# Performance work log

Hardware: AMD Instinct MI355X
Metric: run time of the kernel (lower is better)

The kernel has to match this reference:

```python
import jax, jax.numpy as jnp
import numpy as np

B, S, N, Q, H, Z = 2, 4096, 256, 64, 8, 512

def _glorot(key, shape):
    fan_in, fan_out = shape[-2], shape[-1]
    limit = np.sqrt(6.0 / (fan_in + fan_out))
    return jax.random.uniform(key, shape, jnp.float32, -limit, limit)

def setup_inputs() -> dict:
    key = jax.random.key(0)
    k0, k1, k2, k3 = jax.random.split(key, 4)
    X = jax.random.normal(k0, (B, S, N), dtype=jnp.float32)
    M = _glorot(k1, (H, N, N))        # stacked per-head bilinear matrices
    W_v = _glorot(k2, (H, N, Q))      # stacked per-head value projections
    W0 = _glorot(k3, (Q * H, Z))      # output projection
    return {"X": X, "M": M, "W_v": W_v, "W0": W0}

def reference(X, M, W_v, W0):
    # scores[b,h,s,t] = (X @ M_h @ X^T)[b,s,t] / q   (source divides by q, not sqrt(q))
    q = W_v.shape[-1]
    XM = jnp.einsum('bsn,hnm->bhsm', X, M)
    scores = jnp.einsum('bhsm,btm->bhst', XM, X) / q      # [B,H,S,S]
    A = jax.nn.softmax(scores, axis=-1)
    V = jnp.einsum('btn,hnq->bhtq', X, W_v)               # [B,H,S,Q]
    Zh = jnp.einsum('bhst,bhtq->bshq', A, V)              # [B,S,H,Q]
    Zc = Zh.reshape(Zh.shape[0], Zh.shape[1], -1)         # concat heads -> [B,S,H*Q]
    return Zc @ W0                                        # [B,S,Z]
```

## Files before the change

kernel.cpp:

```cpp
#include <hip/hip_runtime.h>

typedef unsigned short u16;
typedef unsigned long long uptr;
typedef __attribute__((ext_vector_type(8))) short bf16x8;
typedef __attribute__((ext_vector_type(4))) float f32x4;
typedef __attribute__((ext_vector_type(16))) float f32x16;

#define MFMA16(a,b,c) __builtin_amdgcn_mfma_f32_16x16x32_bf16((a),(b),(c),0,0,0)
#define MFMA32(a,b,c) __builtin_amdgcn_mfma_f32_32x32x16_bf16((a),(b),(c),0,0,0)

#define BB 2
#define SS 4096
#define NN 256
#define HH 8
#define QQ 64
#define ZZ 512

__device__ __forceinline__ u16 f2bf(float f){
  unsigned int u = __float_as_uint(f);
  u += 0x7fffu + ((u >> 16) & 1u);
  return (u16)(u >> 16);
}

__device__ __forceinline__ f32x4 fzero(){ f32x4 z = {0.f,0.f,0.f,0.f}; return z; }

__device__ __forceinline__ f32x16 zero16(){
  f32x16 z;
  #pragma unroll
  for (int i = 0; i < 16; i++) z[i] = 0.f;
  return z;
}

__device__ __forceinline__ unsigned pkbf(float a, float b){
  unsigned r;
  asm("v_cvt_pk_bf16_f32 %0, %1, %2" : "=v"(r) : "v"(a), "v"(b));
  return r;
}

typedef __attribute__((address_space(1))) const void gas_void;
typedef __attribute__((address_space(3))) void las_void;
__device__ __forceinline__ void gload16(const void* g, void* l){
  __builtin_amdgcn_global_load_lds((gas_void*)(uptr)g,
                                   (las_void*)(uptr)(unsigned)(uptr)l, 16, 0, 0);
}

__device__ __forceinline__ void do_transpose(const float* __restrict__ ip,
                                             u16* __restrict__ op, int R, int C,
                                             int bx, int by, float (*t)[33], int tid){
  int c0 = bx * 32, r0 = by * 32;
  int c = tid & 31, r = tid >> 5;
  #pragma unroll
  for (int rr = 0; rr < 32; rr += 8)
    t[r + rr][c] = ip[(size_t)(r0 + r + rr) * C + (c0 + c)];
  __syncthreads();
  #pragma unroll
  for (int rr = 0; rr < 32; rr += 8)
    op[(size_t)(c0 + r + rr) * R + (r0 + c)] = f2bf(t[c][r + rr]);
}

__global__ __launch_bounds__(256) void prep_kernel(const float* __restrict__ X,
                                                   const float* __restrict__ M,
                                                   const float* __restrict__ Wv,
                                                   const float* __restrict__ W0,
                                                   u16* __restrict__ Kb,
                                                   u16* __restrict__ Mq,
                                                   u16* __restrict__ Wvt,
                                                   u16* __restrict__ W0t){
  __shared__ float t[32][33];
  int bid = blockIdx.x, tid = threadIdx.x;
  if (bid < 2048){
    int i = bid * 256 + tid;
    float4 v = ((const float4*)X)[i];
    ushort4 o;
    o.x = f2bf(v.x); o.y = f2bf(v.y); o.z = f2bf(v.z); o.w = f2bf(v.w);
    ((ushort4*)Kb)[i] = o;
    return;
  }
  int b2 = bid - 2048;
  if (b2 < 64){
    int h = b2 >> 3, ct = b2 & 7;
    const float* Msrc = M + (size_t)h * NN * NN;
    u16* dst = Mq + (size_t)(h * 8 + ct) * 8192;
    #pragma unroll
    for (int rep = 0; rep < 4; rep++){
      int p = rep * 256 + tid;
      int kk = p >> 6, lane = p & 63;
      int l31 = lane & 31, hi = lane >> 5;
      const float* s = Msrc + (size_t)(kk * 16 + hi * 8) * NN + ct * 32 + l31;
      union { u16 u[8]; uint4 v; } tmp;
      #pragma unroll
      for (int j = 0; j < 8; j++) tmp.u[j] = f2bf(s[(size_t)j * NN]);
      *(uint4*)(dst + (size_t)p * 8) = tmp.v;
    }
    return;
  }
  if (b2 < 192){
    int b3 = b2 - 64;
    int bz = b3 >> 4, by = (b3 >> 1) & 7, bx = b3 & 1;
    do_transpose(Wv + (size_t)bz * NN * QQ, Wvt + (size_t)bz * NN * QQ, NN, QQ, bx, by, t, tid);
  } else {
    int b4 = b2 - 192;
    int by = b4 >> 4, bx = b4 & 15;
    do_transpose(W0, W0t, ZZ, ZZ, bx, by, t, tid);
  }
}

__global__ __launch_bounds__(256) void vt_kernel(const u16* __restrict__ Xb,
                                                 const u16* __restrict__ Wvt,
                                                 u16* __restrict__ Vt){
  int bh = blockIdx.y, b = bh >> 3, h = bh & 7;
  int tbase = blockIdx.x * 256;
  int lane = threadIdx.x & 63, w = threadIdx.x >> 6;
  int lr = lane & 15, g = lane >> 4, lk = g * 8;

  const u16* Ap = Wvt + ((size_t)h * QQ + w * 16 + lr) * NN + lk;
  bf16x8 afr[8];
  #pragma unroll
  for (int ks = 0; ks < 8; ks++) afr[ks] = *(const bf16x8*)(Ap + 32 * ks);

  f32x4 acc[16];
  #pragma unroll
  for (int n = 0; n < 16; n++) acc[n] = fzero();

  for (int n = 0; n < 16; n++){
    const u16* bp = Xb + ((size_t)b * SS + tbase + n * 16 + lr) * NN + lk;
    #pragma unroll
    for (int ks = 0; ks < 8; ks++)
      acc[n] = MFMA16(afr[ks], *(const bf16x8*)(bp + 32 * ks), acc[n]);
  }
  u16* Op = Vt + ((size_t)bh * QQ + w * 16 + g * 4) * SS + tbase;
  #pragma unroll
  for (int n = 0; n < 16; n++)
    #pragma unroll
    for (int r = 0; r < 4; r++)
      Op[(size_t)r * SS + n * 16 + lr] = f2bf(acc[n][r]);
}

__global__ __launch_bounds__(256, 2) void attn_kernel(const u16* __restrict__ Mq,
                                                      const u16* __restrict__ Kb,
                                                      const u16* __restrict__ Vt,
                                                      u16* __restrict__ Zc){
  int lid = blockIdx.x;
  int bh = (lid & 7) | (((lid >> 3) & 1) << 3);
  int qi = lid >> 4;
  int b = bh >> 3, h = bh & 7;

  int tid = threadIdx.x, lane = tid & 63, w = tid >> 6;
  int l31 = lane & 31, hi = lane >> 5;
  int hi16 = hi * 16;
  int sw = (lane & 7) << 4;

  __shared__ u16 k_lds[2 * 64 * 256];
  __shared__ u16 v_lds[2 * 64 * 64];
  char* kl = (char*)k_lds;
  char* vl = (char*)v_lds;

  int qrow = qi * 128 + w * 32 + l31;

  const char* Kg = (const char*)(Kb + (size_t)b * SS * NN);
  const char* Vg = (const char*)(Vt + (size_t)bh * QQ * SS);

  int koffK[8], koffV[2];
  #pragma unroll
  for (int c = 0; c < 8; c++){
    int x = c * 4096 + w * 1024 + lane * 16;
    koffK[c] = x ^ (((x >> 9) & 7) << 4);
  }
  #pragma unroll
  for (int c = 0; c < 2; c++){
    int x = c * 4096 + w * 1024 + lane * 16;
    int vq = x >> 7, ko = x & 127;
    koffV[c] = vq * 8192 + (ko ^ ((vq & 7) << 4));
  }
  int kOff[16], vOff[4];
  #pragma unroll
  for (int ks = 0; ks < 16; ks++) kOff[ks] = l31 * 512 + ((ks * 32 + hi16) ^ sw);
  #pragma unroll
  for (int c = 0; c < 4; c++) vOff[c] = l31 * 128 + ((c * 32 + hi16) ^ sw);

#define STAGE(kt_, CUR_) do {                                              \
    const char* kg_ = Kg + (size_t)(kt_) * 32768;                          \
    const char* vg_ = Vg + (size_t)(kt_) * 128;                            \
    _Pragma("unroll")                                                      \
    for (int c = 0; c < 8; c++)                                            \
      gload16(kg_ + koffK[c], kl + (CUR_) * 32768 + c * 4096 + w * 1024);  \
    _Pragma("unroll")                                                      \
    for (int c = 0; c < 2; c++)                                            \
      gload16(vg_ + koffV[c], vl + (CUR_) * 8192 + c * 4096 + w * 1024);   \
  } while (0)

  STAGE(0, 0);

  bf16x8 qfr[16];
  {
    const float QSCALE = 0.015625f * 1.4426950408889634f;
    const u16* Xp = Kb + ((size_t)b * SS + qrow) * NN + hi * 8;
    bf16x8 xfr[16];
    #pragma unroll
    for (int kk = 0; kk < 16; kk++) xfr[kk] = *(const bf16x8*)(Xp + kk * 16);
    const u16* Mqh = Mq + (size_t)(h * 8) * 8192 + (size_t)lane * 8;
    #pragma unroll
    for (int ct = 0; ct < 8; ct++){
      f32x16 acc = zero16();
      const u16* ap = Mqh + (size_t)ct * 8192;
      #pragma unroll
      for (int kk = 0; kk < 16; kk++)
        acc = MFMA32(*(const bf16x8*)(ap + kk * 512), xfr[kk], acc);
      #pragma unroll
      for (int i = 0; i < 16; i++) acc[i] *= QSCALE;
      {
        unsigned a0 = pkbf(acc[0], acc[1]),  b0 = pkbf(acc[2], acc[3]);
        unsigned c0 = pkbf(acc[4], acc[5]),  d0 = pkbf(acc[6], acc[7]);
        asm("v_permlane32_swap_b32 %0, %1" : "+v"(a0), "+v"(c0));
        asm("v_permlane32_swap_b32 %0, %1" : "+v"(b0), "+v"(d0));
        union { bf16x8 v; unsigned u[4]; } u0;
        u0.u[0] = a0; u0.u[1] = b0; u0.u[2] = c0; u0.u[3] = d0;
        qfr[2 * ct] = u0.v;
      }
      {
        unsigned a1 = pkbf(acc[8], acc[9]),   b1 = pkbf(acc[10], acc[11]);
        unsigned c1 = pkbf(acc[12], acc[13]), d1 = pkbf(acc[14], acc[15]);
        asm("v_permlane32_swap_b32 %0, %1" : "+v"(a1), "+v"(c1));
        asm("v_permlane32_swap_b32 %0, %1" : "+v"(b1), "+v"(d1));
        union { bf16x8 v; unsigned u[4]; } u1;
        u1.u[0] = a1; u1.u[1] = b1; u1.u[2] = c1; u1.u[3] = d1;
        qfr[2 * ct + 1] = u1.v;
      }
    }
  }

  f32x16 o0 = zero16(), o1 = zero16();
  float m = -1e30f, l = 0.f;

#define PVSTEP(P, RB, VOFF, VCONST) do {                                   \
    unsigned a_ = pkbf(P[RB+0], P[RB+1]);                                  \
    unsigned b_ = pkbf(P[RB+2], P[RB+3]);                                  \
    unsigned c_ = pkbf(P[RB+4], P[RB+5]);                                  \
    unsigned d_ = pkbf(P[RB+6], P[RB+7]);                                  \
    asm("v_permlane32_swap_b32 %0, %1" : "+v"(a_), "+v"(c_));              \
    asm("v_permlane32_swap_b32 %0, %1" : "+v"(b_), "+v"(d_));              \
    union { bf16x8 v; unsigned u[4]; } pu_;                                \
    pu_.u[0] = a_; pu_.u[1] = b_; pu_.u[2] = c_; pu_.u[3] = d_;            \
    bf16x8 vf0_ = *(const bf16x8*)(vl + (VOFF) + (VCONST));                \
    bf16x8 vf1_ = *(const bf16x8*)(vl + (VOFF) + (VCONST) + 4096);         \
    o0 = MFMA32(pu_.v, vf0_, o0);                                          \
    o1 = MFMA32(pu_.v, vf1_, o1);                                          \
  } while (0)

#define ITER(kt_, CUR_, LAST_) do {                                        \
    if (!(LAST_)) STAGE((kt_) + 1, (CUR_) ^ 1);                            \
    if (LAST_) { asm volatile("s_waitcnt vmcnt(0)" ::: "memory"); }        \
    else       { asm volatile("s_waitcnt vmcnt(10)" ::: "memory"); }       \
    __builtin_amdgcn_sched_barrier(0);                                     \
    __builtin_amdgcn_s_barrier();                                          \
    __builtin_amdgcn_sched_barrier(0);                                     \
    f32x16 p0 = zero16(), p1 = zero16();                                   \
    __builtin_amdgcn_s_setprio(1);                                         \
    _Pragma("unroll")                                                      \
    for (int ks = 0; ks < 16; ks++){                                       \
      bf16x8 k0 = *(const bf16x8*)(kl + (CUR_) * 32768 + kOff[ks]);        \
      bf16x8 k1 = *(const bf16x8*)(kl + (CUR_) * 32768 + kOff[ks] + 16384);\
      p0 = MFMA32(k0, qfr[ks], p0);                                        \
      p1 = MFMA32(k1, qfr[ks], p1);                                        \
    }                                                                      \
    __builtin_amdgcn_s_setprio(0);                                         \
      \
    float r_[16];                                                          \
    _Pragma("unroll")                                                      \
    for (int i = 0; i < 16; i++) r_[i] = fmaxf(p0[i], p1[i]);              \
    _Pragma("unroll")                                                      \
    for (int i = 0; i < 8; i++) r_[i] = fmaxf(r_[i], r_[i + 8]);           \
    _Pragma("unroll")                                                      \
    for (int i = 0; i < 4; i++) r_[i] = fmaxf(r_[i], r_[i + 4]);           \
    float pm = fmaxf(fmaxf(r_[0], r_[1]), fmaxf(r_[2], r_[3]));            \
    pm = fmaxf(pm, __shfl_xor(pm, 32));                                    \
    if (__any(pm > m + 8.0f)){                        \
      float mn_ = fmaxf(m, pm);                                            \
      float fs_ = exp2f(m - mn_);                                          \
      m = mn_; l *= fs_;                                                   \
      _Pragma("unroll")                                                    \
      for (int i = 0; i < 16; i++){                                        \
        int q_ = (i & 3) + 8 * (i >> 2) + 4 * hi;                          \
        float fv_ = __int_as_float(__builtin_amdgcn_ds_bpermute(           \
                        q_ << 2, __float_as_int(fs_)));                    \
        o0[i] *= fv_; o1[i] *= fv_;                                        \
      }                                                                    \
    }                                                                      \
    _Pragma("unroll")                                                      \
    for (int i = 0; i < 16; i++){                                          \
      p0[i] = exp2f(p0[i] - m);                                            \
      p1[i] = exp2f(p1[i] - m);                                            \
    }                                                                      \
    { float s_[16];                                                        \
      _Pragma("unroll")                                                    \
      for (int i = 0; i < 16; i++) s_[i] = p0[i] + p1[i];                  \
      _Pragma("unroll")                                                    \
      for (int i = 0; i < 8; i++) s_[i] += s_[i + 8];                      \
      _Pragma("unroll")                                                    \
      for (int i = 0; i < 4; i++) s_[i] += s_[i + 4];                      \
      float ps_ = (s_[0] + s_[1]) + (s_[2] + s_[3]);                       \
      ps_ += __shfl_xor(ps_, 32);                                          \
      l += ps_; }                                                          \
    __builtin_amdgcn_s_setprio(1);                                         \
    PVSTEP(p0, 0, vOff[0], (CUR_) * 8192);                                 \
    PVSTEP(p0, 8, vOff[1], (CUR_) * 8192);                                 \
    PVSTEP(p1, 0, vOff[2], (CUR_) * 8192);                                 \
    PVSTEP(p1, 8, vOff[3], (CUR_) * 8192);                                 \
    __builtin_amdgcn_s_setprio(0);                                         \
    __builtin_amdgcn_s_barrier();                                          \
    __builtin_amdgcn_sched_barrier(0);                                     \
  } while (0)

  for (int kt2 = 0; kt2 < 31; kt2++){
    ITER(2 * kt2,     0, 0);
    ITER(2 * kt2 + 1, 1, 0);
  }
  ITER(62, 0, 0);
  ITER(63, 1, 1);
#undef ITER
#undef PVSTEP
#undef STAGE

  float inv = 1.0f / l;
  u16* Op = Zc + ((size_t)b * SS + qi * 128 + w * 32) * (HH * QQ) + h * QQ;
  #pragma unroll
  for (int i = 0; i < 16; i++){
    int q = (i & 3) + 8 * (i >> 2) + 4 * hi;
    float fv = __int_as_float(__builtin_amdgcn_ds_bpermute(q << 2, __float_as_int(inv)));
    u16* row = Op + (size_t)q * (HH * QQ);
    row[l31]      = f2bf(o0[i] * fv);
    row[32 + l31] = f2bf(o1[i] * fv);
  }
}

__global__ __launch_bounds__(256) void out_kernel(const u16* __restrict__ Zc,
                                                  const u16* __restrict__ W0t,
                                                  float* __restrict__ out){
  int rbase = blockIdx.x * 64, cbase = blockIdx.y * 128;
  int lane = threadIdx.x & 63, w = threadIdx.x >> 6;
  int lr = lane & 15, g = lane >> 4, lk = g * 8;

  const u16* Ap = Zc + (size_t)(rbase + w * 16 + lr) * ZZ + lk;
  f32x4 acc[8];
  #pragma unroll
  for (int n = 0; n < 8; n++) acc[n] = fzero();

  for (int ks = 0; ks < 16; ks++){
    bf16x8 afr = *(const bf16x8*)(Ap + 32 * ks);
    #pragma unroll
    for (int n = 0; n < 8; n++){
      const u16* bp = W0t + (size_t)(cbase + n * 16 + lr) * ZZ + lk + 32 * ks;
      acc[n] = MFMA16(afr, *(const bf16x8*)bp, acc[n]);
    }
  }
  float* Op = out + (size_t)(rbase + w * 16 + g * 4) * ZZ + cbase;
  #pragma unroll
  for (int n = 0; n < 8; n++)
    #pragma unroll
    for (int r = 0; r < 4; r++)
      Op[(size_t)r * ZZ + n * 16 + lr] = acc[n][r];
}

extern "C" void kernel_launch(void* const* d_in, const int* in_sizes, int n_in,
                              void* d_out, int out_size, void* d_ws, size_t ws_size,
                              hipStream_t stream){
  (void)in_sizes; (void)n_in; (void)out_size; (void)ws_size;
  const float* X  = (const float*)d_in[0];
  const float* M  = (const float*)d_in[1];
  const float* Wv = (const float*)d_in[2];
  const float* W0 = (const float*)d_in[3];
  float* out = (float*)d_out;

  char* ws = (char*)d_ws;
  size_t off = 0;
  auto alloc = [&](size_t bytes) -> void* {
    void* p = ws + off; off += (bytes + 255) & ~(size_t)255; return p;
  };
  u16* Kb  = (u16*)alloc((size_t)BB * SS * NN * 2);
  u16* Vtb = (u16*)alloc((size_t)BB * HH * QQ * SS * 2);
  u16* Mq  = (u16*)alloc((size_t)HH * NN * NN * 2);
  u16* Wvt = (u16*)alloc((size_t)HH * QQ * NN * 2);
  u16* W0t = (u16*)alloc((size_t)ZZ * ZZ * 2);
  u16* Zc  = (u16*)alloc((size_t)BB * SS * HH * QQ * 2);

  prep_kernel<<<dim3(2496), dim3(256), 0, stream>>>(X, M, Wv, W0, Kb, Mq, Wvt, W0t);
  vt_kernel<<<dim3(SS/256, BB*HH), dim3(256), 0, stream>>>(Kb, Wvt, Vtb);
  attn_kernel<<<dim3(512), dim3(256), 0, stream>>>(Mq, Kb, Vtb, Zc);
  out_kernel<<<dim3(BB*SS/64, ZZ/128), dim3(256), 0, stream>>>(Zc, W0t, out);
}
```

Baseline: 344.5 us.

## Shrink attention blocks, drop double buffering, stage operands through LDS

The attention kernel moves to 128-thread blocks covering 64 query rows with a single-buffered K/V LDS tile. The grid doubles to 1024 blocks and up to four blocks may share a CU. Loads now wait on vmcnt(0) before compute and the next tile is issued only after the compute finishes, so load latency is no longer overlapped within a block. vt_kernel and out_kernel now stage their X/Zc tiles into swizzled LDS with async global-to-LDS loads instead of reading fragments directly from global memory, and vt_kernel uses half the rows per block.

```diff
diff --git a/kernel.cpp b/kernel.cpp
--- a/kernel.cpp
+++ b/kernel.cpp
@@ -108,35 +108,51 @@
 __global__ __launch_bounds__(256) void vt_kernel(const u16* __restrict__ Xb,
                                                  const u16* __restrict__ Wvt,
                                                  u16* __restrict__ Vt){
+  __shared__ u16 x_lds[128 * 256];
   int bh = blockIdx.y, b = bh >> 3, h = bh & 7;
-  int tbase = blockIdx.x * 256;
-  int lane = threadIdx.x & 63, w = threadIdx.x >> 6;
+  int tbase = blockIdx.x * 128;
+  int tid = threadIdx.x;
+  int lane = tid & 63, w = tid >> 6;
   int lr = lane & 15, g = lane >> 4, lk = g * 8;
+
+  const char* src = (const char*)(Xb + ((size_t)b * SS + tbase) * NN);
+  #pragma unroll
+  for (int c = 0; c < 16; c++){
+    int x = c * 4096 + tid * 16;
+    gload16(src + (x ^ (((x >> 9) & 7) << 4)), (char*)x_lds + x);
+  }
 
   const u16* Ap = Wvt + ((size_t)h * QQ + w * 16 + lr) * NN + lk;
   bf16x8 afr[8];
   #pragma unroll
   for (int ks = 0; ks < 8; ks++) afr[ks] = *(const bf16x8*)(Ap + 32 * ks);
 
-  f32x4 acc[16];
-  #pragma unroll
-  for (int n = 0; n < 16; n++) acc[n] = fzero();
-
-  for (int n = 0; n < 16; n++){
-    const u16* bp = Xb + ((size_t)b * SS + tbase + n * 16 + lr) * NN + lk;
-    #pragma unroll
-    for (int ks = 0; ks < 8; ks++)
-      acc[n] = MFMA16(afr[ks], *(const bf16x8*)(bp + 32 * ks), acc[n]);
+  asm volatile("s_waitcnt vmcnt(0)" ::: "memory");
+  __syncthreads();
+
+  f32x4 acc[8];
+  #pragma unroll
+  for (int n = 0; n < 8; n++) acc[n] = fzero();
+
+  #pragma unroll
+  for (int n = 0; n < 8; n++){
+    int row = n * 16 + lr;
+    int rb = row * 512, swr = (row & 7) << 4;
+    #pragma unroll
+    for (int ks = 0; ks < 8; ks++){
+      bf16x8 xf = *(const bf16x8*)((const char*)x_lds + ((rb + lk * 2 + 64 * ks) ^ swr));
+      acc[n] = MFMA16(afr[ks], xf, acc[n]);
+    }
   }
   u16* Op = Vt + ((size_t)bh * QQ + w * 16 + g * 4) * SS + tbase;
   #pragma unroll
-  for (int n = 0; n < 16; n++)
+  for (int n = 0; n < 8; n++)
     #pragma unroll
     for (int r = 0; r < 4; r++)
       Op[(size_t)r * SS + n * 16 + lr] = f2bf(acc[n][r]);
 }
 
-__global__ __launch_bounds__(256, 2) void attn_kernel(const u16* __restrict__ Mq,
+__global__ __launch_bounds__(128, 4) void attn_kernel(const u16* __restrict__ Mq,
                                                       const u16* __restrict__ Kb,
                                                       const u16* __restrict__ Vt,
                                                       u16* __restrict__ Zc){
@@ -150,25 +166,25 @@
   int hi16 = hi * 16;
   int sw = (lane & 7) << 4;
 
-  __shared__ u16 k_lds[2 * 64 * 256];
-  __shared__ u16 v_lds[2 * 64 * 64];
+  __shared__ u16 k_lds[64 * 256];
+  __shared__ u16 v_lds[64 * 64];
   char* kl = (char*)k_lds;
   char* vl = (char*)v_lds;
 
-  int qrow = qi * 128 + w * 32 + l31;
+  int qrow = qi * 64 + w * 32 + l31;
 
   const char* Kg = (const char*)(Kb + (size_t)b * SS * NN);
   const char* Vg = (const char*)(Vt + (size_t)bh * QQ * SS);
 
-  int koffK[8], koffV[2];
-  #pragma unroll
-  for (int c = 0; c < 8; c++){
-    int x = c * 4096 + w * 1024 + lane * 16;
+  int koffK[16], koffV[4];
+  #pragma unroll
+  for (int c = 0; c < 16; c++){
+    int x = c * 2048 + tid * 16;
     koffK[c] = x ^ (((x >> 9) & 7) << 4);
   }
   #pragma unroll
-  for (int c = 0; c < 2; c++){
-    int x = c * 4096 + w * 1024 + lane * 16;
+  for (int c = 0; c < 4; c++){
+    int x = c * 2048 + tid * 16;
     int vq = x >> 7, ko = x & 127;
     koffV[c] = vq * 8192 + (ko ^ ((vq & 7) << 4));
   }
@@ -178,18 +194,18 @@
   #pragma unroll
   for (int c = 0; c < 4; c++) vOff[c] = l31 * 128 + ((c * 32 + hi16) ^ sw);
 
-#define STAGE(kt_, CUR_) do {                                              \
+#define STAGE(kt_) do {                                                    \
     const char* kg_ = Kg + (size_t)(kt_) * 32768;                          \
     const char* vg_ = Vg + (size_t)(kt_) * 128;                            \
     _Pragma("unroll")                                                      \
-    for (int c = 0; c < 8; c++)                                            \
-      gload16(kg_ + koffK[c], kl + (CUR_) * 32768 + c * 4096 + w * 1024);  \
-    _Pragma("unroll")                                                      \
-    for (int c = 0; c < 2; c++)                                            \
-      gload16(vg_ + koffV[c], vl + (CUR_) * 8192 + c * 4096 + w * 1024);   \
+    for (int c = 0; c < 16; c++)                                           \
+      gload16(kg_ + koffK[c], kl + c * 2048 + tid * 16);                   \
+    _Pragma("unroll")                                                      \
+    for (int c = 0; c < 4; c++)                                            \
+      gload16(vg_ + koffV[c], vl + c * 2048 + tid * 16);                   \
   } while (0)
 
-  STAGE(0, 0);
+  STAGE(0);
 
   bf16x8 qfr[16];
   {
@@ -232,7 +248,7 @@
   f32x16 o0 = zero16(), o1 = zero16();
   float m = -1e30f, l = 0.f;
 
-#define PVSTEP(P, RB, VOFF, VCONST) do {                                   \
+#define PVSTEP(P, RB, VOFF) do {                                           \
     unsigned a_ = pkbf(P[RB+0], P[RB+1]);                                  \
     unsigned b_ = pkbf(P[RB+2], P[RB+3]);                                  \
     unsigned c_ = pkbf(P[RB+4], P[RB+5]);                                  \
@@ -241,16 +257,14 @@
     asm("v_permlane32_swap_b32 %0, %1" : "+v"(b_), "+v"(d_));              \
     union { bf16x8 v; unsigned u[4]; } pu_;                                \
     pu_.u[0] = a_; pu_.u[1] = b_; pu_.u[2] = c_; pu_.u[3] = d_;            \
-    bf16x8 vf0_ = *(const bf16x8*)(vl + (VOFF) + (VCONST));                \
-    bf16x8 vf1_ = *(const bf16x8*)(vl + (VOFF) + (VCONST) + 4096);         \
+    bf16x8 vf0_ = *(const bf16x8*)(vl + (VOFF));                           \
+    bf16x8 vf1_ = *(const bf16x8*)(vl + (VOFF) + 4096);                    \
     o0 = MFMA32(pu_.v, vf0_, o0);                                          \
     o1 = MFMA32(pu_.v, vf1_, o1);                                          \
   } while (0)
 
-#define ITER(kt_, CUR_, LAST_) do {                                        \
-    if (!(LAST_)) STAGE((kt_) + 1, (CUR_) ^ 1);                            \
-    if (LAST_) { asm volatile("s_waitcnt vmcnt(0)" ::: "memory"); }        \
-    else       { asm volatile("s_waitcnt vmcnt(10)" ::: "memory"); }       \
+#define ITER() do {                                                        \
+    asm volatile("s_waitcnt vmcnt(0)" ::: "memory");                       \
     __builtin_amdgcn_sched_barrier(0);                                     \
     __builtin_amdgcn_s_barrier();                                          \
     __builtin_amdgcn_sched_barrier(0);                                     \
@@ -258,8 +272,8 @@
     __builtin_amdgcn_s_setprio(1);                                         \
     _Pragma("unroll")                                                      \
     for (int ks = 0; ks < 16; ks++){                                       \
-      bf16x8 k0 = *(const bf16x8*)(kl + (CUR_) * 32768 + kOff[ks]);        \
-      bf16x8 k1 = *(const bf16x8*)(kl + (CUR_) * 32768 + kOff[ks] + 16384);\
+      bf16x8 k0 = *(const bf16x8*)(kl + kOff[ks]);                         \
+      bf16x8 k1 = *(const bf16x8*)(kl + kOff[ks] + 16384);                 \
       p0 = MFMA32(k0, qfr[ks], p0);                                        \
       p1 = MFMA32(k1, qfr[ks], p1);                                        \
     }                                                                      \
@@ -302,27 +316,25 @@
       ps_ += __shfl_xor(ps_, 32);                                          \
       l += ps_; }                                                          \
     __builtin_amdgcn_s_setprio(1);                                         \
-    PVSTEP(p0, 0, vOff[0], (CUR_) * 8192);                                 \
-    PVSTEP(p0, 8, vOff[1], (CUR_) * 8192);                                 \
-    PVSTEP(p1, 0, vOff[2], (CUR_) * 8192);                                 \
-    PVSTEP(p1, 8, vOff[3], (CUR_) * 8192);                                 \
+    PVSTEP(p0, 0, vOff[0]);                                                \
+    PVSTEP(p0, 8, vOff[1]);                                                \
+    PVSTEP(p1, 0, vOff[2]);                                                \
+    PVSTEP(p1, 8, vOff[3]);                                                \
     __builtin_amdgcn_s_setprio(0);                                         \
     __builtin_amdgcn_s_barrier();                                          \
     __builtin_amdgcn_sched_barrier(0);                                     \
   } while (0)
 
-  for (int kt2 = 0; kt2 < 31; kt2++){
-    ITER(2 * kt2,     0, 0);
-    ITER(2 * kt2 + 1, 1, 0);
-  }
-  ITER(62, 0, 0);
-  ITER(63, 1, 1);
+  for (int kt = 0; kt < SS / 64; ++kt){
+    ITER();
+    if (kt < SS / 64 - 1) STAGE(kt + 1);
+  }
 #undef ITER
 #undef PVSTEP
 #undef STAGE
 
   float inv = 1.0f / l;
-  u16* Op = Zc + ((size_t)b * SS + qi * 128 + w * 32) * (HH * QQ) + h * QQ;
+  u16* Op = Zc + ((size_t)b * SS + qi * 64 + w * 32) * (HH * QQ) + h * QQ;
   #pragma unroll
   for (int i = 0; i < 16; i++){
     int q = (i & 3) + 8 * (i >> 2) + 4 * hi;
@@ -336,17 +348,30 @@
 __global__ __launch_bounds__(256) void out_kernel(const u16* __restrict__ Zc,
                                                   const u16* __restrict__ W0t,
                                                   float* __restrict__ out){
+  __shared__ u16 a_lds[64 * 512];
   int rbase = blockIdx.x * 64, cbase = blockIdx.y * 128;
-  int lane = threadIdx.x & 63, w = threadIdx.x >> 6;
+  int tid = threadIdx.x;
+  int lane = tid & 63, w = tid >> 6;
   int lr = lane & 15, g = lane >> 4, lk = g * 8;
 
-  const u16* Ap = Zc + (size_t)(rbase + w * 16 + lr) * ZZ + lk;
+  const char* src = (const char*)(Zc + (size_t)rbase * ZZ);
+  #pragma unroll
+  for (int c = 0; c < 16; c++){
+    int x = c * 4096 + tid * 16;
+    gload16(src + (x ^ (((x >> 10) & 7) << 4)), (char*)a_lds + x);
+  }
+  asm volatile("s_waitcnt vmcnt(0)" ::: "memory");
+  __syncthreads();
+
+  int arow = w * 16 + lr;
+  int arb = arow * 1024, asw = (arow & 7) << 4;
+
   f32x4 acc[8];
   #pragma unroll
   for (int n = 0; n < 8; n++) acc[n] = fzero();
 
   for (int ks = 0; ks < 16; ks++){
-    bf16x8 afr = *(const bf16x8*)(Ap + 32 * ks);
+    bf16x8 afr = *(const bf16x8*)((const char*)a_lds + ((arb + lk * 2 + 64 * ks) ^ asw));
     #pragma unroll
     for (int n = 0; n < 8; n++){
       const u16* bp = W0t + (size_t)(cbase + n * 16 + lr) * ZZ + lk + 32 * ks;
@@ -384,7 +409,7 @@
   u16* Zc  = (u16*)alloc((size_t)BB * SS * HH * QQ * 2);
 
   prep_kernel<<<dim3(2496), dim3(256), 0, stream>>>(X, M, Wv, W0, Kb, Mq, Wvt, W0t);
-  vt_kernel<<<dim3(SS/256, BB*HH), dim3(256), 0, stream>>>(Kb, Wvt, Vtb);
-  attn_kernel<<<dim3(512), dim3(256), 0, stream>>>(Mq, Kb, Vtb, Zc);
+  vt_kernel<<<dim3(SS/128, BB*HH), dim3(256), 0, stream>>>(Kb, Wvt, Vtb);
+  attn_kernel<<<dim3(1024), dim3(128), 0, stream>>>(Mq, Kb, Vtb, Zc);
   out_kernel<<<dim3(BB*SS/64, ZZ/128), dim3(256), 0, stream>>>(Zc, W0t, out);
 }
```

Result: slower. 436.9 us (+26.8%).
